# Kernel tuning notes

Hardware: AMD Instinct MI355X
Metric: run time of the kernel (lower is better)

## Reference

```python
import jax, jax.numpy as jnp
import numpy as np


def setup_inputs() -> dict:
    key = jax.random.key(0)
    k1, k2, k3 = jax.random.split(key, 3)
    B, H, L, D = 4, 16, 1024, 64
    q = jax.random.normal(k1, (B, H, L, D), dtype=jnp.float32)
    k = jax.random.normal(k2, (B, H, L, D), dtype=jnp.float32)
    attn_mask = jax.random.randint(k3, (B, H, L, L), 0, 2).astype(bool)
    return {"q": q, "k": k, "attn_mask": attn_mask}


def reference(q, k, attn_mask):
    # q, k: [B, H, L, D]. The original builds a [B,H,L,D,L] tensor
    # c[b,h,i,m,j] = exp(-(q[b,h,i,m]-k[b,h,j,m])^2), then for each dim m
    # keeps only the entries where rank of q[i,m] (along seq) equals rank of
    # k[j,m], scatters them into an LxL grid and averages over m.
    # Equivalent fused form: sort q and k per dimension, pair equal ranks,
    # and scatter-add exp(-(q_sorted - k_sorted)^2)/D into p[b,h,i,j].
    B, H, L, D = q.shape
    q_idx = jnp.argsort(q, axis=2)                       # [B,H,L,D] int
    k_idx = jnp.argsort(k, axis=2)
    q_sorted = jnp.take_along_axis(q, q_idx, axis=2)     # [B,H,L,D]
    k_sorted = jnp.take_along_axis(k, k_idx, axis=2)
    diff = q_sorted - k_sorted
    vals = jnp.exp(-(diff * diff))                       # [B,H,L,D]
    # linear index into the flattened [L,L] grid, plus batch*head offset
    lin = q_idx * L + k_idx                              # [B,H,L,D]
    bh_off = (jnp.arange(B * H) * (L * L)).reshape(B, H, 1, 1)
    flat_idx = (lin + bh_off).ravel()
    p = jnp.zeros(B * H * L * L, dtype=q.dtype).at[flat_idx].add(vals.ravel())
    p = (p / D).reshape(B, H, L, L)
    return jnp.where(attn_mask, jnp.zeros((), dtype=p.dtype), p)
```

## Files before the change

### kernel.cpp

```cpp
#include <hip/hip_runtime.h>
#include <stdint.h>
#include <string.h>


#define LL 1024
#define DD 64
#define NBH 64
#define PAIRS_BYTES ((size_t)NBH * DD * LL * 4)

__device__ __forceinline__ uint32_t f2ord(float x) {
    uint32_t u = __float_as_uint(x);
    return (u & 0x80000000u) ? ~u : (u | 0x80000000u);
}
__device__ __forceinline__ float ord2f(uint32_t o) {
    uint32_t u = (o & 0x80000000u) ? (o & 0x7fffffffu) : ~o;
    return __uint_as_float(u);
}

__global__ __launch_bounds__(256) void swd3_detect(
    const uint32_t* __restrict__ mw, uint32_t* __restrict__ flags)
{
    __shared__ int sm[256];
    const int t = threadIdx.x;
    int any = 0;
    for (int i = t; i < 8192; i += 256) any |= (mw[i] > 1u) ? 1 : 0;
    sm[t] = any;
    __syncthreads();
    for (int o = 128; o > 0; o >>= 1) {
        if (t < o) sm[t] |= sm[t + o];
        __syncthreads();
    }
    if (t == 0) flags[1] = sm[0] ? 1u : 0u;
}

__global__ __launch_bounds__(512) void swd3_phase1(
    const float* __restrict__ q, const float* __restrict__ k,
    uint32_t* __restrict__ pairs)
{
    __shared__ alignas(16) uint64_t sq[LL];
    __shared__ alignas(16) uint64_t sk[LL];

    const int raw  = blockIdx.x;
    const int slot = raw >> 3;
    const int bh   = (raw & 7) * 8 + (slot >> 6);
    const int d    = slot & 63;
    const int t    = threadIdx.x;

    const size_t colbase = (size_t)bh * (LL * DD) + d;
    uint64_t xq0, xq1, xk0, xk1;
    {
        const uint32_t e0 = 2u * t, e1 = 2u * t + 1u;
        xq0 = ((uint64_t)f2ord(q[colbase + (size_t)e0 * DD]) << 32) | e0;
        xq1 = ((uint64_t)f2ord(q[colbase + (size_t)e1 * DD]) << 32) | e1;
        xk0 = ((uint64_t)f2ord(k[colbase + (size_t)e0 * DD]) << 32) | e0;
        xk1 = ((uint64_t)f2ord(k[colbase + (size_t)e1 * DD]) << 32) | e1;
    }

    auto shfl64 = [&](uint64_t v, int m) -> uint64_t {
        const uint32_t lo = __shfl_xor((uint32_t)v, m);
        const uint32_t hi = __shfl_xor((uint32_t)(v >> 32), m);
        return ((uint64_t)hi << 32) | lo;
    };
    auto shfl_step = [&](int m, bool up) {
        const bool keepmin = (((t & m) == 0) == up);
        uint64_t y;
        y = shfl64(xq0, m); xq0 = keepmin ? (xq0 < y ? xq0 : y) : (xq0 > y ? xq0 : y);
        y = shfl64(xq1, m); xq1 = keepmin ? (xq1 < y ? xq1 : y) : (xq1 > y ? xq1 : y);
        y = shfl64(xk0, m); xk0 = keepmin ? (xk0 < y ? xk0 : y) : (xk0 > y ? xk0 : y);
        y = shfl64(xk1, m); xk1 = keepmin ? (xk1 < y ? xk1 : y) : (xk1 > y ? xk1 : y);
    };
    auto internal_step = [&](bool up) {
        uint64_t lo, hi;
        lo = xq0 < xq1 ? xq0 : xq1; hi = xq0 > xq1 ? xq0 : xq1;
        xq0 = up ? lo : hi; xq1 = up ? hi : lo;
        lo = xk0 < xk1 ? xk0 : xk1; hi = xk0 > xk1 ? xk0 : xk1;
        xk0 = up ? lo : hi; xk1 = up ? hi : lo;
    };
    auto lds_step = [&](int j, int k2) {
        const int r = t & (j - 1);
        const int a = ((t ^ r) << 1) | r;
        const int b = a | j;
        const bool upl = ((a & k2) == 0);
        uint64_t xa = sq[a], xb = sq[b];
        if ((xa > xb) == upl) { sq[a] = xb; sq[b] = xa; }
        xa = sk[a]; xb = sk[b];
        if ((xa > xb) == upl) { sk[a] = xb; sk[b] = xa; }
        __syncthreads();
    };
    auto store_regs = [&]() {
        sq[2 * t] = xq0; sq[2 * t + 1] = xq1;
        sk[2 * t] = xk0; sk[2 * t + 1] = xk1;
        __syncthreads();
    };
    auto load_regs = [&]() {
        xq0 = sq[2 * t]; xq1 = sq[2 * t + 1];
        xk0 = sk[2 * t]; xk1 = sk[2 * t + 1];
    };

    #pragma unroll
    for (int lk = 1; lk <= 7; ++lk) {
        const int k2 = 1 << lk;
        const bool up = ((t & (k2 >> 1)) == 0);
        #pragma unroll
        for (int m = k2 >> 2; m >= 1; m >>= 1) shfl_step(m, up);
        internal_step(up);
    }
    {
        const bool up = ((t & 128) == 0);
        store_regs();
        lds_step(128, 256);
        load_regs();
        #pragma unroll
        for (int m = 32; m >= 1; m >>= 1) shfl_step(m, up);
        internal_step(up);
    }
    {
        const bool up = ((t & 256) == 0);
        store_regs();
        lds_step(256, 512);
        lds_step(128, 512);
        load_regs();
        #pragma unroll
        for (int m = 32; m >= 1; m >>= 1) shfl_step(m, up);
        internal_step(up);
    }
    {
        store_regs();
        lds_step(512, 1024);
        lds_step(256, 1024);
        lds_step(128, 1024);
        load_regs();
        #pragma unroll
        for (int m = 32; m >= 1; m >>= 1) shfl_step(m, true);
        internal_step(true);
    }

    __syncthreads();
    uint32_t* pr = (uint32_t*)sq;
    {
        uint32_t iq = (uint32_t)xq0 & 1023u, ik = (uint32_t)xk0 & 1023u;
        float df = ord2f((uint32_t)(xq0 >> 32)) - ord2f((uint32_t)(xk0 >> 32));
        float val = __expf(-df * df) * (1.0f / 64.0f);
        pr[iq] = (__float_as_uint(val) & 0xFFFFFC00u) | ik;
        iq = (uint32_t)xq1 & 1023u; ik = (uint32_t)xk1 & 1023u;
        df = ord2f((uint32_t)(xq1 >> 32)) - ord2f((uint32_t)(xk1 >> 32));
        val = __expf(-df * df) * (1.0f / 64.0f);
        pr[iq] = (__float_as_uint(val) & 0xFFFFFC00u) | ik;
    }
    __syncthreads();

    uint32_t* pp = pairs + ((size_t)bh * DD + d) * LL;
    pp[t]       = pr[t];
    pp[t + 512] = pr[t + 512];
}

__global__ __launch_bounds__(256) void swd3_phase2(
    const uint32_t* __restrict__ pairs, const void* __restrict__ maskp,
    const uint32_t* __restrict__ flags, float* __restrict__ out)
{
    __shared__ float acc[8 * LL];

    const int bh = blockIdx.x >> 7;
    const int s  = blockIdx.x & 127;
    const int i0 = s * 8;
    const int t  = threadIdx.x;

    float4* acc4 = (float4*)acc;
    #pragma unroll
    for (int v = 0; v < 8; ++v)
        acc4[v * 256 + t] = make_float4(0.f, 0.f, 0.f, 0.f);
    __syncthreads();

    const uint32_t* pb = pairs + (size_t)bh * (DD * LL);
    #pragma unroll
    for (int it = 0; it < 2; ++it) {
        const int idx = it * 256 + t;
        const int dd = idx >> 3;
        const int ii = idx & 7;
        const uint32_t pv = pb[dd * LL + i0 + ii];
        const float val = __uint_as_float(pv & 0xFFFFFC00u);
        const int  ik  = (int)(pv & 1023u);
        atomicAdd(&acc[ii * LL + ik], val);
    }
    __syncthreads();

    const size_t cellbase = ((size_t)bh << 20) + ((size_t)i0 << 10);
    const bool mask_byte = (flags[1] != 0u);
    float* ob = out + cellbase;

    #pragma unroll
    for (int v = 0; v < 8; ++v) {
        const int p = v * 256 + t;
        const float4 a = acc4[p];
        int mx, my, mz, mw2;
        if (mask_byte) {
            const uchar4 m = ((const uchar4*)((const uint8_t*)maskp + cellbase))[p];
            mx = m.x; my = m.y; mz = m.z; mw2 = m.w;
        } else {
            const int4 m = ((const int4*)((const int32_t*)maskp + cellbase))[p];
            mx = m.x; my = m.y; mz = m.z; mw2 = m.w;
        }
        float4 r;
        r.x = mx  ? 0.f : a.x;
        r.y = my  ? 0.f : a.y;
        r.z = mz  ? 0.f : a.z;
        r.w = mw2 ? 0.f : a.w;
        ((float4*)ob)[p] = r;
    }
}

extern "C" void kernel_launch(void* const* d_in, const int* in_sizes, int n_in,
                              void* d_out, int out_size, void* d_ws, size_t ws_size,
                              hipStream_t stream) {
    const float* q = (const float*)d_in[0];
    const float* k = (const float*)d_in[1];
    const void* mask = d_in[2];
    uint32_t* pairs = (uint32_t*)d_ws;
    uint32_t* flags = (uint32_t*)((char*)d_ws + PAIRS_BYTES);

    const bool ws_ok = (ws_size >= PAIRS_BYTES + 256);
    hipError_t e1 = hipSuccess, e2 = hipSuccess, e3 = hipSuccess;
    (void)hipGetLastError();

    if (ws_ok) {
        swd3_detect<<<1, 256, 0, stream>>>((const uint32_t*)mask, flags);
        e1 = hipGetLastError();
        swd3_phase1<<<NBH * DD, 512, 0, stream>>>(q, k, pairs);
        e2 = hipGetLastError();
        swd3_phase2<<<NBH * 128, 256, 0, stream>>>(pairs, mask, flags, (float*)d_out);
        e3 = hipGetLastError();
    }

    if (!ws_ok || e1 != hipSuccess || e2 != hipSuccess || e3 != hipSuccess) {
        static float h_stamp[8];
        h_stamp[0] = !ws_ok ? (9000.0f + (float)(ws_size >> 20))
                            : (1000.0f + (float)(int)e1);
        h_stamp[1] = 2000.0f + (float)(int)e2;
        h_stamp[2] = 3000.0f + (float)(int)e3;
        h_stamp[3] = h_stamp[0];
        hipMemcpyAsync(d_out, h_stamp, sizeof(h_stamp),
                       hipMemcpyHostToDevice, stream);
    }
}
```

Baseline: 581.4 us.

## Sort four elements per thread in phase1 and use nontemporal masked stores in phase2

The phase1 bitonic sort now runs with 256 threads, each holding four keys instead of two. Two stages move from shuffles and LDS into register compare-exchanges, which removes one LDS round trip and some barriers. The pairs write-out and the phase2 pair loads are vectorized, and phase2 now uses nontemporal loads for the mask and nontemporal stores for the output to avoid polluting the cache with streaming data. The cost is more register pressure per thread and less parallelism within each block.

Measured after the change: 558.7 us. 3.9% less time.

```diff
diff --git a/kernel.cpp b/kernel.cpp
--- a/kernel.cpp
+++ b/kernel.cpp
@@ -7,6 +7,11 @@
 #define DD 64
 #define NBH 64
 #define PAIRS_BYTES ((size_t)NBH * DD * LL * 4)
+
+typedef float    vf4   __attribute__((ext_vector_type(4)));
+typedef uint32_t vu4   __attribute__((ext_vector_type(4)));
+typedef int32_t  vi4   __attribute__((ext_vector_type(4)));
+typedef unsigned long long vu64x2 __attribute__((ext_vector_type(2)));
 
 __device__ __forceinline__ uint32_t f2ord(float x) {
     uint32_t u = __float_as_uint(x);
@@ -33,7 +38,7 @@
     if (t == 0) flags[1] = sm[0] ? 1u : 0u;
 }
 
-__global__ __launch_bounds__(512) void swd3_phase1(
+__global__ __launch_bounds__(256) void swd3_phase1(
     const float* __restrict__ q, const float* __restrict__ k,
     uint32_t* __restrict__ pairs)
 {
@@ -47,15 +52,19 @@
     const int t    = threadIdx.x;
 
     const size_t colbase = (size_t)bh * (LL * DD) + d;
-    uint64_t xq0, xq1, xk0, xk1;
-    {
-        const uint32_t e0 = 2u * t, e1 = 2u * t + 1u;
-        xq0 = ((uint64_t)f2ord(q[colbase + (size_t)e0 * DD]) << 32) | e0;
-        xq1 = ((uint64_t)f2ord(q[colbase + (size_t)e1 * DD]) << 32) | e1;
-        xk0 = ((uint64_t)f2ord(k[colbase + (size_t)e0 * DD]) << 32) | e0;
-        xk1 = ((uint64_t)f2ord(k[colbase + (size_t)e1 * DD]) << 32) | e1;
-    }
-
+    uint64_t xq[4], xk[4];
+    #pragma unroll
+    for (int s = 0; s < 4; ++s) {
+        const uint32_t e = 4u * t + s;
+        xq[s] = ((uint64_t)f2ord(q[colbase + (size_t)e * DD]) << 32) | e;
+        xk[s] = ((uint64_t)f2ord(k[colbase + (size_t)e * DD]) << 32) | e;
+    }
+
+    auto cex = [](uint64_t& a, uint64_t& b, bool up) {
+        const uint64_t lo = a < b ? a : b;
+        const uint64_t hi = a < b ? b : a;
+        a = up ? lo : hi; b = up ? hi : lo;
+    };
     auto shfl64 = [&](uint64_t v, int m) -> uint64_t {
         const uint32_t lo = __shfl_xor((uint32_t)v, m);
         const uint32_t hi = __shfl_xor((uint32_t)(v >> 32), m);
@@ -63,149 +72,160 @@
     };
     auto shfl_step = [&](int m, bool up) {
         const bool keepmin = (((t & m) == 0) == up);
-        uint64_t y;
-        y = shfl64(xq0, m); xq0 = keepmin ? (xq0 < y ? xq0 : y) : (xq0 > y ? xq0 : y);
-        y = shfl64(xq1, m); xq1 = keepmin ? (xq1 < y ? xq1 : y) : (xq1 > y ? xq1 : y);
-        y = shfl64(xk0, m); xk0 = keepmin ? (xk0 < y ? xk0 : y) : (xk0 > y ? xk0 : y);
-        y = shfl64(xk1, m); xk1 = keepmin ? (xk1 < y ? xk1 : y) : (xk1 > y ? xk1 : y);
-    };
-    auto internal_step = [&](bool up) {
-        uint64_t lo, hi;
-        lo = xq0 < xq1 ? xq0 : xq1; hi = xq0 > xq1 ? xq0 : xq1;
-        xq0 = up ? lo : hi; xq1 = up ? hi : lo;
-        lo = xk0 < xk1 ? xk0 : xk1; hi = xk0 > xk1 ? xk0 : xk1;
-        xk0 = up ? lo : hi; xk1 = up ? hi : lo;
+        #pragma unroll
+        for (int s = 0; s < 4; ++s) {
+            uint64_t y = shfl64(xq[s], m);
+            xq[s] = keepmin ? (xq[s] < y ? xq[s] : y) : (xq[s] > y ? xq[s] : y);
+            y = shfl64(xk[s], m);
+            xk[s] = keepmin ? (xk[s] < y ? xk[s] : y) : (xk[s] > y ? xk[s] : y);
+        }
+    };
+    auto internal2 = [&](bool up) {
+        cex(xq[0], xq[2], up); cex(xq[1], xq[3], up);
+        cex(xk[0], xk[2], up); cex(xk[1], xk[3], up);
+    };
+    auto internal1 = [&](bool up) {
+        cex(xq[0], xq[1], up); cex(xq[2], xq[3], up);
+        cex(xk[0], xk[1], up); cex(xk[2], xk[3], up);
     };
     auto lds_step = [&](int j, int k2) {
-        const int r = t & (j - 1);
-        const int a = ((t ^ r) << 1) | r;
-        const int b = a | j;
-        const bool upl = ((a & k2) == 0);
-        uint64_t xa = sq[a], xb = sq[b];
-        if ((xa > xb) == upl) { sq[a] = xb; sq[b] = xa; }
-        xa = sk[a]; xb = sk[b];
-        if ((xa > xb) == upl) { sk[a] = xb; sk[b] = xa; }
+        #pragma unroll
+        for (int h = 0; h < 2; ++h) {
+            const int v = t + h * 256;
+            const int r = v & (j - 1);
+            const int a = ((v ^ r) << 1) | r;
+            const int b = a | j;
+            const bool upl = ((a & k2) == 0);
+            uint64_t xa = sq[a], xb = sq[b];
+            if ((xa > xb) == upl) { sq[a] = xb; sq[b] = xa; }
+            xa = sk[a]; xb = sk[b];
+            if ((xa > xb) == upl) { sk[a] = xb; sk[b] = xa; }
+        }
         __syncthreads();
     };
     auto store_regs = [&]() {
-        sq[2 * t] = xq0; sq[2 * t + 1] = xq1;
-        sk[2 * t] = xk0; sk[2 * t + 1] = xk1;
+        vu64x2* q2 = (vu64x2*)sq;
+        vu64x2* k2p = (vu64x2*)sk;
+        vu64x2 v;
+        v.x = xq[0]; v.y = xq[1]; q2[2 * t] = v;
+        v.x = xq[2]; v.y = xq[3]; q2[2 * t + 1] = v;
+        v.x = xk[0]; v.y = xk[1]; k2p[2 * t] = v;
+        v.x = xk[2]; v.y = xk[3]; k2p[2 * t + 1] = v;
         __syncthreads();
     };
     auto load_regs = [&]() {
-        xq0 = sq[2 * t]; xq1 = sq[2 * t + 1];
-        xk0 = sk[2 * t]; xk1 = sk[2 * t + 1];
-    };
-
-    #pragma unroll
-    for (int lk = 1; lk <= 7; ++lk) {
+        const vu64x2* q2 = (const vu64x2*)sq;
+        const vu64x2* k2p = (const vu64x2*)sk;
+        vu64x2 v;
+        v = q2[2 * t];     xq[0] = v.x; xq[1] = v.y;
+        v = q2[2 * t + 1]; xq[2] = v.x; xq[3] = v.y;
+        v = k2p[2 * t];     xk[0] = v.x; xk[1] = v.y;
+        v = k2p[2 * t + 1]; xk[2] = v.x; xk[3] = v.y;
+    };
+
+    cex(xq[0], xq[1], true);  cex(xq[2], xq[3], false);
+    cex(xk[0], xk[1], true);  cex(xk[2], xk[3], false);
+    { const bool up = ((t & 1) == 0); internal2(up); internal1(up); }
+    #pragma unroll
+    for (int lk = 3; lk <= 8; ++lk) {
         const int k2 = 1 << lk;
-        const bool up = ((t & (k2 >> 1)) == 0);
-        #pragma unroll
-        for (int m = k2 >> 2; m >= 1; m >>= 1) shfl_step(m, up);
-        internal_step(up);
+        const bool up = ((t & (k2 >> 2)) == 0);
+        #pragma unroll
+        for (int m = k2 >> 3; m >= 1; m >>= 1) shfl_step(m, up);
+        internal2(up); internal1(up);
     }
     {
         const bool up = ((t & 128) == 0);
         store_regs();
-        lds_step(128, 256);
+        lds_step(256, 512);
         load_regs();
         #pragma unroll
         for (int m = 32; m >= 1; m >>= 1) shfl_step(m, up);
-        internal_step(up);
-    }
-    {
-        const bool up = ((t & 256) == 0);
-        store_regs();
-        lds_step(256, 512);
-        lds_step(128, 512);
-        load_regs();
-        #pragma unroll
-        for (int m = 32; m >= 1; m >>= 1) shfl_step(m, up);
-        internal_step(up);
+        internal2(up); internal1(up);
     }
     {
         store_regs();
         lds_step(512, 1024);
         lds_step(256, 1024);
-        lds_step(128, 1024);
         load_regs();
         #pragma unroll
         for (int m = 32; m >= 1; m >>= 1) shfl_step(m, true);
-        internal_step(true);
+        internal2(true); internal1(true);
     }
 
     __syncthreads();
     uint32_t* pr = (uint32_t*)sq;
-    {
-        uint32_t iq = (uint32_t)xq0 & 1023u, ik = (uint32_t)xk0 & 1023u;
-        float df = ord2f((uint32_t)(xq0 >> 32)) - ord2f((uint32_t)(xk0 >> 32));
-        float val = __expf(-df * df) * (1.0f / 64.0f);
+    #pragma unroll
+    for (int s = 0; s < 4; ++s) {
+        const uint32_t iq = (uint32_t)xq[s] & 1023u;
+        const uint32_t ik = (uint32_t)xk[s] & 1023u;
+        const float df = ord2f((uint32_t)(xq[s] >> 32))
+                       - ord2f((uint32_t)(xk[s] >> 32));
+        const float val = __expf(-df * df) * (1.0f / 64.0f);
         pr[iq] = (__float_as_uint(val) & 0xFFFFFC00u) | ik;
-        iq = (uint32_t)xq1 & 1023u; ik = (uint32_t)xk1 & 1023u;
-        df = ord2f((uint32_t)(xq1 >> 32)) - ord2f((uint32_t)(xk1 >> 32));
-        val = __expf(-df * df) * (1.0f / 64.0f);
-        pr[iq] = (__float_as_uint(val) & 0xFFFFFC00u) | ik;
-    }
-    __syncthreads();
-
-    uint32_t* pp = pairs + ((size_t)bh * DD + d) * LL;
-    pp[t]       = pr[t];
-    pp[t + 512] = pr[t + 512];
+    }
+    __syncthreads();
+
+    vu4* pp4 = (vu4*)(pairs + ((size_t)bh * DD + d) * LL);
+    pp4[t] = ((const vu4*)pr)[t];
 }
 
 __global__ __launch_bounds__(256) void swd3_phase2(
     const uint32_t* __restrict__ pairs, const void* __restrict__ maskp,
     const uint32_t* __restrict__ flags, float* __restrict__ out)
 {
-    __shared__ float acc[8 * LL];
+    __shared__ alignas(16) float acc[8 * LL];
 
     const int bh = blockIdx.x >> 7;
     const int s  = blockIdx.x & 127;
     const int i0 = s * 8;
     const int t  = threadIdx.x;
 
-    float4* acc4 = (float4*)acc;
-    #pragma unroll
-    for (int v = 0; v < 8; ++v)
-        acc4[v * 256 + t] = make_float4(0.f, 0.f, 0.f, 0.f);
-    __syncthreads();
-
-    const uint32_t* pb = pairs + (size_t)bh * (DD * LL);
-    #pragma unroll
-    for (int it = 0; it < 2; ++it) {
-        const int idx = it * 256 + t;
-        const int dd = idx >> 3;
-        const int ii = idx & 7;
-        const uint32_t pv = pb[dd * LL + i0 + ii];
-        const float val = __uint_as_float(pv & 0xFFFFFC00u);
-        const int  ik  = (int)(pv & 1023u);
-        atomicAdd(&acc[ii * LL + ik], val);
+    vf4* acc4 = (vf4*)acc;
+    #pragma unroll
+    for (int v = 0; v < 8; ++v) {
+        vf4 z; z.x = 0.f; z.y = 0.f; z.z = 0.f; z.w = 0.f;
+        acc4[v * 256 + t] = z;
+    }
+    __syncthreads();
+
+    {
+        const uint32_t* pb = pairs + (size_t)bh * (DD * LL);
+        const int dd = t >> 2;
+        const uint2 pv = ((const uint2*)(pb + dd * LL + i0))[t & 3];
+        const int ii0 = 2 * (t & 3), ii1 = ii0 + 1;
+        atomicAdd(&acc[ii0 * LL + (int)(pv.x & 1023u)],
+                  __uint_as_float(pv.x & 0xFFFFFC00u));
+        atomicAdd(&acc[ii1 * LL + (int)(pv.y & 1023u)],
+                  __uint_as_float(pv.y & 0xFFFFFC00u));
     }
     __syncthreads();
 
     const size_t cellbase = ((size_t)bh << 20) + ((size_t)i0 << 10);
     const bool mask_byte = (flags[1] != 0u);
-    float* ob = out + cellbase;
+    vf4* ob = (vf4*)(out + cellbase);
 
     #pragma unroll
     for (int v = 0; v < 8; ++v) {
         const int p = v * 256 + t;
-        const float4 a = acc4[p];
+        const vf4 a = acc4[p];
         int mx, my, mz, mw2;
         if (mask_byte) {
-            const uchar4 m = ((const uchar4*)((const uint8_t*)maskp + cellbase))[p];
-            mx = m.x; my = m.y; mz = m.z; mw2 = m.w;
+            const uint32_t m = __builtin_nontemporal_load(
+                (const uint32_t*)maskp + (cellbase >> 2) + p);
+            mx = (int)(m & 0xFFu); my = (int)((m >> 8) & 0xFFu);
+            mz = (int)((m >> 16) & 0xFFu); mw2 = (int)(m >> 24);
         } else {
-            const int4 m = ((const int4*)((const int32_t*)maskp + cellbase))[p];
+            const vi4 m = __builtin_nontemporal_load(
+                (const vi4*)((const int32_t*)maskp + cellbase) + p);
             mx = m.x; my = m.y; mz = m.z; mw2 = m.w;
         }
-        float4 r;
+        vf4 r;
         r.x = mx  ? 0.f : a.x;
         r.y = my  ? 0.f : a.y;
         r.z = mz  ? 0.f : a.z;
         r.w = mw2 ? 0.f : a.w;
-        ((float4*)ob)[p] = r;
+        __builtin_nontemporal_store(r, ob + p);
     }
 }
 
@@ -225,7 +245,7 @@
     if (ws_ok) {
         swd3_detect<<<1, 256, 0, stream>>>((const uint32_t*)mask, flags);
         e1 = hipGetLastError();
-        swd3_phase1<<<NBH * DD, 512, 0, stream>>>(q, k, pairs);
+        swd3_phase1<<<NBH * DD, 256, 0, stream>>>(q, k, pairs);
         e2 = hipGetLastError();
         swd3_phase2<<<NBH * 128, 256, 0, stream>>>(pairs, mask, flags, (float*)d_out);
         e3 = hipGetLastError();
```
